# Performance work log

Hardware: AMD Instinct MI355X
Metric: run time of the kernel (lower is better)

## Reference

```python
import jax, jax.numpy as jnp
import numpy as np

VOCAB, EMB, HID, LABELS, SEQ = 30522, 768, 1024, 2, 4096


def setup_inputs() -> dict:
    key = jax.random.key(0)
    ks = jax.random.split(key, 8)
    s = 0.02  # keep gate pre-activations in a sane range
    return {
        "sentence": jax.random.randint(ks[0], (SEQ,), 0, VOCAB),
        "emb": jax.random.normal(ks[1], (VOCAB, EMB), jnp.float32),
        "w_ih": jax.random.normal(ks[2], (4 * HID, EMB), jnp.float32) * s,
        "w_hh": jax.random.normal(ks[3], (4 * HID, HID), jnp.float32) * s,
        "b_ih": jax.random.normal(ks[4], (4 * HID,), jnp.float32) * s,
        "b_hh": jax.random.normal(ks[5], (4 * HID,), jnp.float32) * s,
        "w_out": jax.random.normal(ks[6], (LABELS, HID), jnp.float32) * s,
        "b_out": jax.random.normal(ks[7], (LABELS,), jnp.float32) * s,
    }


def reference(sentence, emb, w_ih, w_hh, b_ih, b_hh, w_out, b_out):
    H = w_hh.shape[1]
    x = emb[sentence]                       # [T, E] frozen embedding lookup
    xg = x @ w_ih.T + (b_ih + b_hh)         # [T, 4H] precompute input-to-gate GEMM

    def cell(carry, xgt):
        h, c = carry
        gates = xgt + w_hh @ h              # [4H]
        i, f, g, o = jnp.split(gates, 4)
        i = jax.nn.sigmoid(i)
        f = jax.nn.sigmoid(f)
        g = jnp.tanh(g)
        o = jax.nn.sigmoid(o)
        c = f * c + i * g
        h = o * jnp.tanh(c)
        return (h, c), None

    h0 = jnp.zeros((H,), x.dtype)
    c0 = jnp.zeros((H,), x.dtype)
    (h_T, _), _ = jax.lax.scan(cell, (h0, c0), xg)
    y = h_T @ w_out.T + b_out               # [label_size]
    return jax.nn.log_softmax(y[None, :], axis=-1)  # [1, label_size]
```

## Files before the change

kernel.cpp:

```cpp
#include <hip/hip_runtime.h>
#include <hip/hip_bf16.h>

#define VOCAB 30522
#define EMB   768
#define HID   1024
#define SEQ   4096
#define NG    4096
#define NWG   128
#define RT    256

static __device__ __forceinline__ unsigned short f32_to_bf16(float f) {
  unsigned u = __float_as_uint(f);
  u = (u + 0x7fffu + ((u >> 16) & 1u)) >> 16;
  return (unsigned short)u;
}

#define BM 64
#define BN 64
#define BK 16

__global__ __launch_bounds__(256) void xg_gemm(
    const int* __restrict__ sent, const float* __restrict__ emb,
    const float* __restrict__ w_ih, const float* __restrict__ b_ih,
    const float* __restrict__ b_hh, __hip_bfloat16* __restrict__ xg) {
  __shared__ float As[BK][BM + 4];
  __shared__ float Bs[BK][BN + 4];
  const int tid = threadIdx.x;
  const int n0 = blockIdx.x * BN;
  const int m0 = blockIdx.y * BM;
  const int tx = tid & 15, ty = tid >> 4;
  const int lr = tid >> 2;
  const int lk = (tid & 3) * 4;

  const int arow = sent[m0 + lr];
  const float* aptr = emb + (size_t)arow * EMB + lk;
  const float* bptr = w_ih + (size_t)(n0 + lr) * EMB + lk;

  float acc[4][4] = {};

  for (int k0 = 0; k0 < EMB; k0 += BK) {
    float4 av = *(const float4*)(aptr + k0);
    float4 bv = *(const float4*)(bptr + k0);
    __syncthreads();
    As[lk + 0][lr] = av.x; As[lk + 1][lr] = av.y;
    As[lk + 2][lr] = av.z; As[lk + 3][lr] = av.w;
    Bs[lk + 0][lr] = bv.x; Bs[lk + 1][lr] = bv.y;
    Bs[lk + 2][lr] = bv.z; Bs[lk + 3][lr] = bv.w;
    __syncthreads();
#pragma unroll
    for (int k = 0; k < BK; ++k) {
      float4 a = *(const float4*)&As[k][ty * 4];
      float4 b = *(const float4*)&Bs[k][tx * 4];
      acc[0][0] = fmaf(a.x, b.x, acc[0][0]); acc[0][1] = fmaf(a.x, b.y, acc[0][1]);
      acc[0][2] = fmaf(a.x, b.z, acc[0][2]); acc[0][3] = fmaf(a.x, b.w, acc[0][3]);
      acc[1][0] = fmaf(a.y, b.x, acc[1][0]); acc[1][1] = fmaf(a.y, b.y, acc[1][1]);
      acc[1][2] = fmaf(a.y, b.z, acc[1][2]); acc[1][3] = fmaf(a.y, b.w, acc[1][3]);
      acc[2][0] = fmaf(a.z, b.x, acc[2][0]); acc[2][1] = fmaf(a.z, b.y, acc[2][1]);
      acc[2][2] = fmaf(a.z, b.z, acc[2][2]); acc[2][3] = fmaf(a.z, b.w, acc[2][3]);
      acc[3][0] = fmaf(a.w, b.x, acc[3][0]); acc[3][1] = fmaf(a.w, b.y, acc[3][1]);
      acc[3][2] = fmaf(a.w, b.z, acc[3][2]); acc[3][3] = fmaf(a.w, b.w, acc[3][3]);
    }
  }

#pragma unroll
  for (int i = 0; i < 4; ++i) {
    int gm = m0 + ty * 4 + i;
#pragma unroll
    for (int j = 0; j < 4; ++j) {
      int gn = n0 + tx * 4 + j;
      float v = acc[i][j] + b_ih[gn] + b_hh[gn];
      xg[(size_t)gm * NG + gn] = __float2bfloat16(v);
    }
  }
}

__global__ __launch_bounds__(RT, 1) void lstm_rec(
    const float* __restrict__ w_hh, const __hip_bfloat16* __restrict__ xg,
    unsigned long long* __restrict__ slots) {
  __shared__ unsigned hl[2][512];

  const int tid  = threadIdx.x;
  const int wg   = blockIdx.x;
  const int lane = tid & 63;
  const int wv   = tid >> 6;
  const int c    = lane;
  const int m    = lane & 1;

  unsigned wu[8][16];
#pragma unroll
  for (int s = 0; s < 8; ++s) {
    const int q = s >> 1, mm = s & 1;
    const int gr = q * HID + wg * 8 + 2 * wv + mm;
    const float* wr = w_hh + (size_t)gr * HID;
#pragma unroll
    for (int k = 0; k < 8; ++k) {
      float2 wv2 = *(const float2*)(wr + 2 * (c + 64 * k));
      wu[s][2 * k]     = __float_as_uint(wv2.x);
      wu[s][2 * k + 1] = __float_as_uint(wv2.y);
    }
  }
#pragma unroll
  for (int s = 0; s < 8; ++s)
#pragma unroll
    for (int k = 0; k < 16; ++k)
      asm volatile("" : "+v"(wu[s][k]));

  float cst = 0.f;

  for (int t = 0; t < SEQ; ++t) {
    float xqv = 0.f;
    if (lane < 8) {
      const int q = lane >> 1;
      xqv = __bfloat162float(
          xg[(size_t)t * NG + q * HID + wg * 8 + 2 * wv + (lane & 1)]);
    }

    const unsigned long long want = (unsigned long long)t;
    unsigned long long* sp = slots + ((t & 1) << 9) + 2 * tid;
    unsigned long long v0, v1;
    for (;;) {
      v0 = __hip_atomic_load(sp,     __ATOMIC_RELAXED, __HIP_MEMORY_SCOPE_AGENT);
      v1 = __hip_atomic_load(sp + 1, __ATOMIC_RELAXED, __HIP_MEMORY_SCOPE_AGENT);
      if (((v0 >> 32) == want) & ((v1 >> 32) == want)) break;
    }
    hl[t & 1][2 * tid]     = (unsigned)v0;
    hl[t & 1][2 * tid + 1] = (unsigned)v1;
    __syncthreads();

    const unsigned* hb = hl[t & 1];
    float hx[8], hy[8];
#pragma unroll
    for (int k = 0; k < 8; ++k) {
      unsigned hw = hb[c + 64 * k];
      hx[k] = __uint_as_float(hw << 16);
      hy[k] = __uint_as_float(hw & 0xffff0000u);
    }

    float acc[8];
#pragma unroll
    for (int s = 0; s < 8; ++s) {
      float a = 0.f;
#pragma unroll
      for (int k = 0; k < 8; ++k) {
        a = fmaf(__uint_as_float(wu[s][2 * k]),     hx[k], a);
        a = fmaf(__uint_as_float(wu[s][2 * k + 1]), hy[k], a);
      }
      acc[s] = a;
    }

#pragma unroll
    for (int M = 1, n = 8; M <= 4; M <<= 1, n >>= 1) {
#pragma unroll
      for (int j = 0; j < 4; ++j) {
        if (j < (n >> 1)) {
          float u  = (lane & M) ? acc[2 * j + 1] : acc[2 * j];
          float u2 = (lane & M) ? acc[2 * j]     : acc[2 * j + 1];
          acc[j] = u + __shfl_xor(u2, M, 64);
        }
      }
    }
    float r = acc[0];
    r += __shfl_xor(r, 8, 64);
    r += __shfl_xor(r, 16, 64);
    r += __shfl_xor(r, 32, 64);

    {
      const int s = lane & 7;
      const bool isg = (s >> 1) == 2;
      float z = r + xqv;
      z = isg ? 2.f * z : z;
      float sg = 1.f / (1.f + __expf(-z));
      r = isg ? fmaf(2.f, sg, -1.f) : sg;
    }

    float i_ = __shfl(r, m,     64);
    float f_ = __shfl(r, 2 + m, 64);
    float g_ = __shfl(r, 4 + m, 64);
    float o_ = __shfl(r, 6 + m, 64);

    cst = fmaf(f_, cst, i_ * g_);
    float th = fmaf(2.f, 1.f / (1.f + __expf(-2.f * cst)), -1.f);
    float hn = o_ * th;

    float hn1 = __shfl(hn, 1, 64);
    if (lane == 0) {
      unsigned payload = ((unsigned)f32_to_bf16(hn1) << 16) | (unsigned)f32_to_bf16(hn);
      unsigned long long pv =
          ((unsigned long long)(unsigned)(t + 1) << 32) | (unsigned long long)payload;
      __hip_atomic_store(slots + (((t + 1) & 1) << 9) + (wg * 4 + wv), pv,
                         __ATOMIC_RELAXED, __HIP_MEMORY_SCOPE_AGENT);
    }
  }
}

__global__ __launch_bounds__(256) void head_kernel(
    const unsigned long long* __restrict__ hslots, const float* __restrict__ w_out,
    const float* __restrict__ b_out, float* __restrict__ out) {
  __shared__ float s0[256], s1[256];
  const int tid = threadIdx.x;
  float p0 = 0.f, p1 = 0.f;
  for (int w = tid; w < 512; w += 256) {
    unsigned pw = (unsigned)hslots[w];
    float h0 = __uint_as_float(pw << 16);
    float h1 = __uint_as_float(pw & 0xffff0000u);
    p0 = fmaf(h0, w_out[2 * w], fmaf(h1, w_out[2 * w + 1], p0));
    p1 = fmaf(h0, w_out[HID + 2 * w], fmaf(h1, w_out[HID + 2 * w + 1], p1));
  }
  s0[tid] = p0; s1[tid] = p1;
  __syncthreads();
  for (int off = 128; off; off >>= 1) {
    if (tid < off) { s0[tid] += s0[tid + off]; s1[tid] += s1[tid + off]; }
    __syncthreads();
  }
  if (tid == 0) {
    float y0 = s0[0] + b_out[0], y1 = s1[0] + b_out[1];
    float mx = fmaxf(y0, y1);
    float lse = mx + logf(expf(y0 - mx) + expf(y1 - mx));
    out[0] = y0 - lse;
    out[1] = y1 - lse;
  }
}

extern "C" void kernel_launch(void* const* d_in, const int* in_sizes, int n_in,
                              void* d_out, int out_size, void* d_ws, size_t ws_size,
                              hipStream_t stream) {
  const int*   sent  = (const int*)d_in[0];
  const float* emb   = (const float*)d_in[1];
  const float* w_ih  = (const float*)d_in[2];
  const float* w_hh  = (const float*)d_in[3];
  const float* b_ih  = (const float*)d_in[4];
  const float* b_hh  = (const float*)d_in[5];
  const float* w_out = (const float*)d_in[6];
  const float* b_out = (const float*)d_in[7];
  float* out = (float*)d_out;

  unsigned long long* slots = (unsigned long long*)d_ws;
  __hip_bfloat16* xg = (__hip_bfloat16*)((char*)d_ws + 16384);

  hipMemsetAsync(d_ws, 0, 16384, stream);

  dim3 ggrid(NG / BN, SEQ / BM);
  xg_gemm<<<ggrid, 256, 0, stream>>>(sent, emb, w_ih, b_ih, b_hh, xg);

  lstm_rec<<<NWG, RT, 0, stream>>>(w_hh, xg, slots);

  head_kernel<<<1, 256, 0, stream>>>(slots, w_out, b_out, out);
}
```

Before: 7.480 ms.

## Pack recurrent weights to bf16 and poll h slots from a single wavefront

The register-resident W_hh slice is packed two bf16 values per register, halving VGPR use per thread at the cost of a shift and a mask in the inner loop, and it lowers weight precision. The spin-wait on the global h-slots now runs in wave 0 only. Each lane polls 8 slots and writes them to LDS, and the other waves wait at the barrier. The aim is less polling traffic on shared cache lines across the 128 persistent workgroups, in exchange for serialising the gather through one wave.

```diff
diff --git a/kernel.cpp b/kernel.cpp
--- a/kernel.cpp
+++ b/kernel.cpp
@@ -86,7 +86,7 @@
   const int c    = lane;
   const int m    = lane & 1;
 
-  unsigned wu[8][16];
+  unsigned wp[8][8];
 #pragma unroll
   for (int s = 0; s < 8; ++s) {
     const int q = s >> 1, mm = s & 1;
@@ -95,15 +95,14 @@
 #pragma unroll
     for (int k = 0; k < 8; ++k) {
       float2 wv2 = *(const float2*)(wr + 2 * (c + 64 * k));
-      wu[s][2 * k]     = __float_as_uint(wv2.x);
-      wu[s][2 * k + 1] = __float_as_uint(wv2.y);
+      wp[s][k] = ((unsigned)f32_to_bf16(wv2.y) << 16) | (unsigned)f32_to_bf16(wv2.x);
     }
   }
 #pragma unroll
   for (int s = 0; s < 8; ++s)
 #pragma unroll
-    for (int k = 0; k < 16; ++k)
-      asm volatile("" : "+v"(wu[s][k]));
+    for (int k = 0; k < 8; ++k)
+      asm volatile("" : "+v"(wp[s][k]));
 
   float cst = 0.f;
 
@@ -115,16 +114,24 @@
           xg[(size_t)t * NG + q * HID + wg * 8 + 2 * wv + (lane & 1)]);
     }
 
-    const unsigned long long want = (unsigned long long)t;
-    unsigned long long* sp = slots + ((t & 1) << 9) + 2 * tid;
-    unsigned long long v0, v1;
-    for (;;) {
-      v0 = __hip_atomic_load(sp,     __ATOMIC_RELAXED, __HIP_MEMORY_SCOPE_AGENT);
-      v1 = __hip_atomic_load(sp + 1, __ATOMIC_RELAXED, __HIP_MEMORY_SCOPE_AGENT);
-      if (((v0 >> 32) == want) & ((v1 >> 32) == want)) break;
-    }
-    hl[t & 1][2 * tid]     = (unsigned)v0;
-    hl[t & 1][2 * tid + 1] = (unsigned)v1;
+    if (wv == 0) {
+      const unsigned long long want = (unsigned long long)t;
+      unsigned long long* sb = slots + ((t & 1) << 9);
+      unsigned long long v[8];
+      for (;;) {
+#pragma unroll
+        for (int k = 0; k < 8; ++k)
+          v[k] = __hip_atomic_load(sb + 64 * k + lane,
+                                   __ATOMIC_RELAXED, __HIP_MEMORY_SCOPE_AGENT);
+        bool ok = true;
+#pragma unroll
+        for (int k = 0; k < 8; ++k) ok &= ((v[k] >> 32) == want);
+        if (ok) break;
+      }
+#pragma unroll
+      for (int k = 0; k < 8; ++k)
+        hl[t & 1][64 * k + lane] = (unsigned)v[k];
+    }
     __syncthreads();
 
     const unsigned* hb = hl[t & 1];
@@ -142,8 +149,9 @@
       float a = 0.f;
 #pragma unroll
       for (int k = 0; k < 8; ++k) {
-        a = fmaf(__uint_as_float(wu[s][2 * k]),     hx[k], a);
-        a = fmaf(__uint_as_float(wu[s][2 * k + 1]), hy[k], a);
+        unsigned w = wp[s][k];
+        a = fmaf(__uint_as_float(w << 16),         hx[k], a);
+        a = fmaf(__uint_as_float(w & 0xffff0000u), hy[k], a);
       }
       acc[s] = a;
     }
```

New measurement: 7.486 ms. About the same (+0.1%).
